# Optimization experiments

Measured on AMD Instinct MI355X. Metric: run time of the kernel, lower is better.

The kernel has to match this reference:

```python
import jax, jax.numpy as jnp
import numpy as np

N_NODES = 100000
N_EDGES = 1600000
D_IN = 128
D_OUT = 128


def setup_inputs() -> dict:
    key = jax.random.key(0)
    k_x, k_e, k_wl, k_bl, k_wr = jax.random.split(key, 5)
    x = jax.random.normal(k_x, (N_NODES, D_IN), dtype=jnp.float32)
    edge_index = jax.random.randint(k_e, (2, N_EDGES), 0, N_NODES, dtype=jnp.int64)
    s = 1.0 / np.sqrt(D_IN)
    W_l = jax.random.uniform(k_wl, (D_OUT, D_IN), minval=-s, maxval=s, dtype=jnp.float32)
    b_l = jax.random.uniform(k_bl, (D_OUT,), minval=-s, maxval=s, dtype=jnp.float32)
    W_r = jax.random.uniform(k_wr, (D_OUT, D_IN), minval=-s, maxval=s, dtype=jnp.float32)
    return {"x": x, "edge_index": edge_index, "W_l": W_l, "b_l": b_l, "W_r": W_r}


def reference(x, edge_index, W_l, b_l, W_r):
    # PyG SAGEConv with mean aggregation:
    #   out = lin_l(mean_{j in N(i)} x_j) + lin_r(x_i), followed by ReLU.
    src, dst = edge_index[0], edge_index[1]
    # gather source features [E, D_IN] and mean-aggregate at destinations
    msg_sum = jax.ops.segment_sum(x[src], dst, num_segments=N_NODES)  # [N, D_IN]
    deg = jax.ops.segment_sum(jnp.ones((edge_index.shape[1],), dtype=x.dtype), dst,
                              num_segments=N_NODES)  # [N]
    agg = msg_sum / jnp.maximum(deg, 1.0)[:, None]  # isolated nodes -> 0
    out = agg @ W_l.T + b_l + x @ W_r.T
    return jax.nn.relu(out)
```

## Files before the change

### kernel.cpp

```cpp
#include <hip/hip_runtime.h>
#include <hip/hip_bf16.h>
#include <cstddef>
#include <cstdint>

#define D 128
#define BCAP 262144
#define BCHUNK 4096
#define SLOTS 64
#define TILE 128
#define XBASE 8192
#define SBCAP 5120
#define GPGMAX 64

typedef __bf16 bf16x8 __attribute__((ext_vector_type(8)));
typedef float  f32x4  __attribute__((ext_vector_type(4)));
typedef float  f32x2  __attribute__((ext_vector_type(2)));

__device__ __forceinline__ unsigned int f2bf(float f) {
    unsigned int u = __float_as_uint(f);
    return (u + 0x7FFFu + ((u >> 16) & 1u)) >> 16;
}

__global__ __launch_bounds__(256) void bucketx_kernel(
    const int* __restrict__ ei, int E, int* __restrict__ bucketCnt,
    int2* __restrict__ buckets, int nbBucket, int nbX,
    const float4* __restrict__ x4, uint2* __restrict__ xb2,
    unsigned int* __restrict__ xg, int nq,
    const float* __restrict__ Wl, const float* __restrict__ Wr,
    const float* __restrict__ bl, unsigned short* __restrict__ bfrag,
    float* __restrict__ biasbuf)
{
    const int bid = blockIdx.x;
    if (bid >= nbBucket) {
        const int xi = bid - nbBucket;
        if (xi < nbX) {
            const int base = xi * 1024 + threadIdx.x;
            #pragma unroll
            for (int k = 0; k < 4; k++) {
                int i = base + k * 256;
                if (i < nq) {
                    float4 v = x4[i];
                    uint2 r;
                    r.x = f2bf(v.x) | (f2bf(v.y) << 16);
                    r.y = f2bf(v.z) | (f2bf(v.w) << 16);
                    xb2[i] = r;
                    int g = 0;
                    g = __builtin_amdgcn_cvt_pk_fp8_f32(v.x, v.y, g, false);
                    g = __builtin_amdgcn_cvt_pk_fp8_f32(v.z, v.w, g, true);
                    xg[(size_t)((i >> 5) + 1) * 32 + (i & 31)] = (unsigned int)g;
                }
            }
        } else {
            int f = (xi - nbX) * 256 + threadIdx.x;
            if (f < 4096) {
                int ct   = f >> 9;
                int q    = (f >> 6) & 7;
                int lane = f & 63;
                int o  = 16 * ct + (lane & 15);
                int kb = 32 * q + (lane >> 4) * 8;
                const float* s = (kb < 128) ? (Wl + (size_t)o * 128 + kb)
                                            : (Wr + (size_t)o * 128 + (kb - 128));
                uint4 u;
                u.x = f2bf(s[0]) | (f2bf(s[1]) << 16);
                u.y = f2bf(s[2]) | (f2bf(s[3]) << 16);
                u.z = f2bf(s[4]) | (f2bf(s[5]) << 16);
                u.w = f2bf(s[6]) | (f2bf(s[7]) << 16);
                reinterpret_cast<uint4*>(bfrag)[f] = u;
                if (f < 128) biasbuf[f] = bl[f];
                if (f < 32)  xg[f] = 0u;
            }
        }
        return;
    }
    __shared__ int cnt[8], base[8], pos[8];
    const int cb  = bid * BCHUNK;
    const int end = min(cb + BCHUNK, E);
    if (threadIdx.x < 8) { cnt[threadIdx.x] = 0; pos[threadIdx.x] = 0; }
    __syncthreads();
    int srcs[16], dsts[16];
    #pragma unroll
    for (int k = 0; k < 16; k++) {
        int e = cb + threadIdx.x + k * 256;
        bool v = e < end;
        srcs[k] = v ? ei[e] : 0;
        dsts[k] = v ? ei[E + e] : -1;
        if (v) atomicAdd(&cnt[(dsts[k] >> 8) & 7], 1);
    }
    __syncthreads();
    if (threadIdx.x < 8)
        base[threadIdx.x] = atomicAdd(&bucketCnt[threadIdx.x], cnt[threadIdx.x]);
    __syncthreads();
    #pragma unroll
    for (int k = 0; k < 16; k++) {
        if (dsts[k] >= 0) {
            int p = (dsts[k] >> 8) & 7;
            int o = base[p] + atomicAdd(&pos[p], 1);
            if (o < BCAP) buckets[(size_t)p * BCAP + o] = make_int2(srcs[k], dsts[k]);
        }
    }
}

__global__ __launch_bounds__(256) void granule_kernel(
    const int2* __restrict__ buckets, const int* __restrict__ bucketCnt,
    int* __restrict__ subCnt, unsigned int* __restrict__ sub, int GPG)
{
    __shared__ int cnt[GPGMAX], base[GPGMAX], posl[GPGMAX];
    const int p = blockIdx.x & 7;
    const int j = blockIdx.x >> 3;
    const int n = min(bucketCnt[p], BCAP);
    const int lo = j * 4096;
    if (lo >= n) return;
    const int hi = min(lo + 4096, n);
    for (int i = threadIdx.x; i < GPG; i += 256) { cnt[i] = 0; posl[i] = 0; }
    __syncthreads();
    const int2* B = buckets + (size_t)p * BCAP;
    int2 e[16]; int gi[16];
    #pragma unroll
    for (int k = 0; k < 16; k++) {
        int i = lo + threadIdx.x + k * 256;
        bool v = i < hi;
        e[k] = v ? B[i] : make_int2(0, 0);
        gi[k] = v ? (e[k].y >> 11) : -1;
        if (v) atomicAdd(&cnt[gi[k]], 1);
    }
    __syncthreads();
    for (int i = threadIdx.x; i < GPG; i += 256)
        base[i] = (cnt[i] > 0) ? atomicAdd(&subCnt[p * GPG + i], cnt[i]) : 0;
    __syncthreads();
    #pragma unroll
    for (int k = 0; k < 16; k++) {
        if (gi[k] >= 0) {
            int pos = base[gi[k]] + atomicAdd(&posl[gi[k]], 1);
            if (pos < SBCAP)
                sub[(size_t)(p * GPG + gi[k]) * SBCAP + pos] =
                    (unsigned int)(e[k].x + 1) | ((unsigned int)(e[k].y & 255) << 20);
        }
    }
}

__global__ __launch_bounds__(256) void csrg_kernel(
    const unsigned int* __restrict__ sub, const int* __restrict__ subCnt,
    int* __restrict__ csr, int* __restrict__ deg, int GPG, int N)
{
    __shared__ int lcnt[256];
    const int g  = blockIdx.x;
    const int p  = g & 7;
    const int gi = g >> 3;
    const int sb = p * GPG + gi;
    const int n  = min(subCnt[sb], SBCAP);
    lcnt[threadIdx.x] = 0;
    __syncthreads();
    const unsigned int* S = sub + (size_t)sb * SBCAP;
    const int nbase = g << 8;
    for (int i = threadIdx.x; i < n; i += 256) {
        unsigned int en = S[i];
        int d8  = (en >> 20) & 255;
        int pos = atomicAdd(&lcnt[d8], 1);
        if (pos < SLOTS)
            csr[(size_t)(nbase + d8) * SLOTS + pos] = (int)(en & 0xFFFFFu);
    }
    __syncthreads();
    int node = nbase + threadIdx.x;
    if (node < N) deg[node] = lcnt[threadIdx.x];
}

__device__ __forceinline__ void gather_issue(
    unsigned int (&vv)[16], int raw, int dl, int half, int sub,
    const unsigned int* __restrict__ xg)
{
    #pragma unroll
    for (int u = 0; u < 16; u++) {
        int slot = 2 * u + half;
        int s = (slot < dl) ? __shfl(raw, slot) : 0;
        vv[u] = xg[(size_t)s * 32 + sub];
    }
}

__device__ __forceinline__ void acc_reduce_write(
    const unsigned int (&vv)[16], int raw, int dl, int dT, int row,
    int half, int sub, const unsigned int* __restrict__ xg, unsigned int* lds)
{
    f32x2 a01 = {0.f, 0.f};
    f32x2 a23 = {0.f, 0.f};
    #pragma unroll
    for (int u = 0; u < 16; u++) {
        a01 += __builtin_amdgcn_cvt_pk_f32_fp8(vv[u], false);
        a23 += __builtin_amdgcn_cvt_pk_f32_fp8(vv[u], true);
    }
    if (dl > 32) {
        #pragma unroll
        for (int u = 0; u < 16; u++) {
            int slot = 32 + 2 * u + half;
            int s = (slot < dl) ? __shfl(raw, slot) : 0;
            unsigned int vt = xg[(size_t)s * 32 + sub];
            a01 += __builtin_amdgcn_cvt_pk_f32_fp8(vt, false);
            a23 += __builtin_amdgcn_cvt_pk_f32_fp8(vt, true);
        }
    }
    a01.x += __shfl_xor(a01.x, 32);
    a01.y += __shfl_xor(a01.y, 32);
    a23.x += __shfl_xor(a23.x, 32);
    a23.y += __shfl_xor(a23.y, 32);
    if (half == 0) {
        float inv = 1.0f / fmaxf((float)dT, 1.0f);
        int ch   = (sub >> 1) ^ (row & 7);
        int bofs = row * 64 + ch * 4 + (sub & 1) * 2;
        lds[bofs]     = f2bf(a01.x * inv) | (f2bf(a01.y * inv) << 16);
        lds[bofs + 1] = f2bf(a23.x * inv) | (f2bf(a23.y * inv) << 16);
    }
}

__global__ __launch_bounds__(512, 4) void gathformer_kernel(
    const int* __restrict__ deg_, const int* __restrict__ csr,
    const unsigned int* __restrict__ xg, const unsigned int* __restrict__ xb,
    const unsigned short* __restrict__ bfrag, const float* __restrict__ biasbuf,
    float* __restrict__ out, int N)
{
    __shared__ unsigned int lds[2 * TILE * 64];

    const int w    = threadIdx.x >> 6;
    const int lane = threadIdx.x & 63;
    const int sub  = lane & 31;
    const int half = lane >> 5;
    const int node0 = blockIdx.x * TILE;

    uint4 xs[4];
    const uint4* xb4 = reinterpret_cast<const uint4*>(xb);
    #pragma unroll
    for (int k = 0; k < 4; k++) {
        int idx = k * 512 + (int)threadIdx.x;
        int row = idx >> 4;
        int gr  = min(node0 + row, N - 1);
        xs[k] = xb4[(size_t)gr * 16 + (idx & 15)];
    }

    const int nb0 = node0 + w * 16;
    int degv = 0;
    if (lane < 16) {
        int nd = nb0 + lane;
        if (nd < N) degv = deg_[nd];
    }
    int r0 = csr[(size_t)min(nb0 + 0, N - 1) * SLOTS + lane];
    int r1 = csr[(size_t)min(nb0 + 1, N - 1) * SLOTS + lane];
    int r2 = csr[(size_t)min(nb0 + 2, N - 1) * SLOTS + lane];

    #pragma unroll
    for (int k = 0; k < 4; k++) {
        int idx = k * 512 + (int)threadIdx.x;
        int row = idx >> 4;
        int cw  = (idx & 15) ^ (row & 7);
        *reinterpret_cast<uint4*>(&lds[XBASE + row * 64 + cw * 4]) = xs[k];
    }

    unsigned int vA[16], vB[16];
    int dl0 = min(__shfl(degv, 0), SLOTS);
    gather_issue(vA, r0, dl0, half, sub, xg);
    #pragma unroll
    for (int i = 0; i < 16; i += 2) {
        int dl1 = min(__shfl(degv, i + 1), SLOTS);
        gather_issue(vB, r1, dl1, half, sub, xg);
        int r3 = (i + 3 < 16) ? csr[(size_t)min(nb0 + i + 3, N - 1) * SLOTS + lane] : 0;
        int dT0 = __shfl(degv, i);
        acc_reduce_write(vA, r0, dl0, dT0, w * 16 + i, half, sub, xg, lds);
        dl0 = (i + 2 < 16) ? min(__shfl(degv, i + 2), SLOTS) : 0;
        if (i + 2 < 16) gather_issue(vA, r2, dl0, half, sub, xg);
        int r4 = (i + 4 < 16) ? csr[(size_t)min(nb0 + i + 4, N - 1) * SLOTS + lane] : 0;
        int dT1 = __shfl(degv, i + 1);
        acc_reduce_write(vB, r1, dl1, dT1, w * 16 + i + 1, half, sub, xg, lds);
        r0 = r2; r1 = r3; r2 = r4;
    }

    const int quad = lane >> 4;
    const int r15  = lane & 15;
    bf16x8 bw[8];
    #pragma unroll
    for (int q = 0; q < 8; q++)
        bw[q] = reinterpret_cast<const bf16x8*>(bfrag)[(w * 8 + q) * 64 + lane];
    const float bias = biasbuf[16 * w + r15];
    const int col = 16 * w + r15;

    __syncthreads();

    #pragma unroll 2
    for (int mt = 0; mt < 8; mt++) {
        int rowbase = node0 + mt * 16;
        if (rowbase >= N) break;
        f32x4 acc = {0.f, 0.f, 0.f, 0.f};
        const int r     = mt * 16 + r15;
        const int rbase = r * 64;
        const int rx    = r & 7;
        #pragma unroll
        for (int q = 0; q < 4; q++) {
            int ch = (quad + 4 * q) ^ rx;
            bf16x8 a = *reinterpret_cast<const bf16x8*>(&lds[rbase + ch * 4]);
            acc = __builtin_amdgcn_mfma_f32_16x16x32_bf16(a, bw[q], acc, 0, 0, 0);
        }
        #pragma unroll
        for (int q = 0; q < 4; q++) {
            int ch = (quad + 4 * q) ^ rx;
            bf16x8 a = *reinterpret_cast<const bf16x8*>(&lds[XBASE + rbase + ch * 4]);
            acc = __builtin_amdgcn_mfma_f32_16x16x32_bf16(a, bw[4 + q], acc, 0, 0, 0);
        }
        #pragma unroll
        for (int rr = 0; rr < 4; rr++) {
            int orow = rowbase + quad * 4 + rr;
            if (orow < N)
                out[(size_t)orow * D + col] = fmaxf(acc[rr] + bias, 0.0f);
        }
    }
}

extern "C" void kernel_launch(void* const* d_in, const int* in_sizes, int n_in,
                              void* d_out, int out_size, void* d_ws, size_t ws_size,
                              hipStream_t stream)
{
    const float* x  = (const float*)d_in[0];
    const int*   ei = (const int*)d_in[1];
    const float* Wl = (const float*)d_in[2];
    const float* bl = (const float*)d_in[3];
    const float* Wr = (const float*)d_in[4];
    float* out = (float*)d_out;

    const int nodes = in_sizes[0] / D;
    const int E     = in_sizes[1] / 2;
    const int NG    = (nodes + 255) >> 8;
    const int GPG   = (NG + 7) >> 3;

    int* deg         = (int*)d_ws;
    unsigned int* xg = (unsigned int*)(deg + nodes);
    int* csr         = (int*)(xg + (size_t)(nodes + 1) * 32);
    unsigned int* xb = (unsigned int*)(csr + (size_t)nodes * SLOTS);
    unsigned short* bfrag = (unsigned short*)(xb + (size_t)nodes * 64);
    float* biasbuf   = (float*)(bfrag + 4096 * 8);
    int* bucketCnt   = (int*)(biasbuf + 128);
    int* subCnt      = bucketCnt + 8;
    int2* buckets    = (int2*)d_out;
    unsigned int* sub = (unsigned int*)((char*)d_out + (size_t)8 * BCAP * 8);

    hipMemsetAsync(bucketCnt, 0, (size_t)(8 + 8 * GPG) * sizeof(int), stream);

    const int nbBucket = (E + BCHUNK - 1) / BCHUNK;
    const int nq  = nodes * 32;
    const int nbX = (nq + 1023) / 1024;
    bucketx_kernel<<<nbBucket + nbX + 16, 256, 0, stream>>>(
        ei, E, bucketCnt, buckets, nbBucket, nbX,
        (const float4*)x, (uint2*)xb, xg, nq, Wl, Wr, bl, bfrag, biasbuf);

    const int PB = (BCAP + 4095) / 4096;
    granule_kernel<<<8 * PB, 256, 0, stream>>>(buckets, bucketCnt, subCnt, sub, GPG);

    csrg_kernel<<<NG, 256, 0, stream>>>(sub, subCnt, csr, deg, GPG, nodes);

    gathformer_kernel<<<(nodes + TILE - 1) / TILE, 512, 0, stream>>>(
        deg, csr, xg, xb, bfrag, biasbuf, out, nodes);
}
```

Before: 221.5 us.

## Replace three-pass bucketed CSR build with direct global-atomic scatter

```diff
diff --git a/kernel.cpp b/kernel.cpp
--- a/kernel.cpp
+++ b/kernel.cpp
@@ -4,13 +4,10 @@
 #include <cstdint>
 
 #define D 128
-#define BCAP 262144
 #define BCHUNK 4096
 #define SLOTS 64
 #define TILE 128
 #define XBASE 8192
-#define SBCAP 5120
-#define GPGMAX 64
 
 typedef __bf16 bf16x8 __attribute__((ext_vector_type(8)));
 typedef float  f32x4  __attribute__((ext_vector_type(4)));
@@ -21,9 +18,9 @@
     return (u + 0x7FFFu + ((u >> 16) & 1u)) >> 16;
 }
 
-__global__ __launch_bounds__(256) void bucketx_kernel(
-    const int* __restrict__ ei, int E, int* __restrict__ bucketCnt,
-    int2* __restrict__ buckets, int nbBucket, int nbX,
+__global__ __launch_bounds__(256) void scatterx_kernel(
+    const int* __restrict__ ei, int E, int* __restrict__ deg,
+    int* __restrict__ csr, int nbScat, int nbX,
     const float4* __restrict__ x4, uint2* __restrict__ xb2,
     unsigned int* __restrict__ xg, int nq,
     const float* __restrict__ Wl, const float* __restrict__ Wr,
@@ -31,8 +28,8 @@
     float* __restrict__ biasbuf)
 {
     const int bid = blockIdx.x;
-    if (bid >= nbBucket) {
-        const int xi = bid - nbBucket;
+    if (bid >= nbScat) {
+        const int xi = bid - nbScat;
         if (xi < nbX) {
             const int base = xi * 1024 + threadIdx.x;
             #pragma unroll
@@ -72,96 +69,23 @@
         }
         return;
     }
-    __shared__ int cnt[8], base[8], pos[8];
-    const int cb  = bid * BCHUNK;
-    const int end = min(cb + BCHUNK, E);
-    if (threadIdx.x < 8) { cnt[threadIdx.x] = 0; pos[threadIdx.x] = 0; }
-    __syncthreads();
+    const int cb = bid * BCHUNK;
     int srcs[16], dsts[16];
     #pragma unroll
     for (int k = 0; k < 16; k++) {
         int e = cb + threadIdx.x + k * 256;
-        bool v = e < end;
+        bool v = e < E;
         srcs[k] = v ? ei[e] : 0;
         dsts[k] = v ? ei[E + e] : -1;
-        if (v) atomicAdd(&cnt[(dsts[k] >> 8) & 7], 1);
-    }
-    __syncthreads();
-    if (threadIdx.x < 8)
-        base[threadIdx.x] = atomicAdd(&bucketCnt[threadIdx.x], cnt[threadIdx.x]);
-    __syncthreads();
+    }
     #pragma unroll
     for (int k = 0; k < 16; k++) {
         if (dsts[k] >= 0) {
-            int p = (dsts[k] >> 8) & 7;
-            int o = base[p] + atomicAdd(&pos[p], 1);
-            if (o < BCAP) buckets[(size_t)p * BCAP + o] = make_int2(srcs[k], dsts[k]);
-        }
-    }
-}
-
-__global__ __launch_bounds__(256) void granule_kernel(
-    const int2* __restrict__ buckets, const int* __restrict__ bucketCnt,
-    int* __restrict__ subCnt, unsigned int* __restrict__ sub, int GPG)
-{
-    __shared__ int cnt[GPGMAX], base[GPGMAX], posl[GPGMAX];
-    const int p = blockIdx.x & 7;
-    const int j = blockIdx.x >> 3;
-    const int n = min(bucketCnt[p], BCAP);
-    const int lo = j * 4096;
-    if (lo >= n) return;
-    const int hi = min(lo + 4096, n);
-    for (int i = threadIdx.x; i < GPG; i += 256) { cnt[i] = 0; posl[i] = 0; }
-    __syncthreads();
-    const int2* B = buckets + (size_t)p * BCAP;
-    int2 e[16]; int gi[16];
-    #pragma unroll
-    for (int k = 0; k < 16; k++) {
-        int i = lo + threadIdx.x + k * 256;
-        bool v = i < hi;
-        e[k] = v ? B[i] : make_int2(0, 0);
-        gi[k] = v ? (e[k].y >> 11) : -1;
-        if (v) atomicAdd(&cnt[gi[k]], 1);
-    }
-    __syncthreads();
-    for (int i = threadIdx.x; i < GPG; i += 256)
-        base[i] = (cnt[i] > 0) ? atomicAdd(&subCnt[p * GPG + i], cnt[i]) : 0;
-    __syncthreads();
-    #pragma unroll
-    for (int k = 0; k < 16; k++) {
-        if (gi[k] >= 0) {
-            int pos = base[gi[k]] + atomicAdd(&posl[gi[k]], 1);
-            if (pos < SBCAP)
-                sub[(size_t)(p * GPG + gi[k]) * SBCAP + pos] =
-                    (unsigned int)(e[k].x + 1) | ((unsigned int)(e[k].y & 255) << 20);
-        }
-    }
-}
-
-__global__ __launch_bounds__(256) void csrg_kernel(
-    const unsigned int* __restrict__ sub, const int* __restrict__ subCnt,
-    int* __restrict__ csr, int* __restrict__ deg, int GPG, int N)
-{
-    __shared__ int lcnt[256];
-    const int g  = blockIdx.x;
-    const int p  = g & 7;
-    const int gi = g >> 3;
-    const int sb = p * GPG + gi;
-    const int n  = min(subCnt[sb], SBCAP);
-    lcnt[threadIdx.x] = 0;
-    __syncthreads();
-    const unsigned int* S = sub + (size_t)sb * SBCAP;
-    const int nbase = g << 8;
-    for (int i = threadIdx.x; i < n; i += 256) {
-        unsigned int en = S[i];
-        int d8  = (en >> 20) & 255;
-        int pos = atomicAdd(&lcnt[d8], 1);
-        if (pos < SLOTS)
-            csr[(size_t)(nbase + d8) * SLOTS + pos] = (int)(en & 0xFFFFFu);
-    }
-    __syncthreads();
-    int node = nbase + threadIdx.x;
-    if (node < N) deg[node] = lcnt[threadIdx.x];
+            int pos = atomicAdd(&deg[dsts[k]], 1);
+            if (pos < SLOTS)
+                csr[(size_t)dsts[k] * SLOTS + pos] = srcs[k] + 1;
+        }
+    }
 }
 
 __device__ __forceinline__ void gather_issue(
@@ -323,8 +247,6 @@
 
     const int nodes = in_sizes[0] / D;
     const int E     = in_sizes[1] / 2;
-    const int NG    = (nodes + 255) >> 8;
-    const int GPG   = (NG + 7) >> 3;
 
     int* deg         = (int*)d_ws;
     unsigned int* xg = (unsigned int*)(deg + nodes);
@@ -332,24 +254,15 @@
     unsigned int* xb = (unsigned int*)(csr + (size_t)nodes * SLOTS);
     unsigned short* bfrag = (unsigned short*)(xb + (size_t)nodes * 64);
     float* biasbuf   = (float*)(bfrag + 4096 * 8);
-    int* bucketCnt   = (int*)(biasbuf + 128);
-    int* subCnt      = bucketCnt + 8;
-    int2* buckets    = (int2*)d_out;
-    unsigned int* sub = (unsigned int*)((char*)d_out + (size_t)8 * BCAP * 8);
-
-    hipMemsetAsync(bucketCnt, 0, (size_t)(8 + 8 * GPG) * sizeof(int), stream);
-
-    const int nbBucket = (E + BCHUNK - 1) / BCHUNK;
+
+    hipMemsetAsync(deg, 0, (size_t)nodes * sizeof(int), stream);
+
+    const int nbScat = (E + BCHUNK - 1) / BCHUNK;
     const int nq  = nodes * 32;
     const int nbX = (nq + 1023) / 1024;
-    bucketx_kernel<<<nbBucket + nbX + 16, 256, 0, stream>>>(
-        ei, E, bucketCnt, buckets, nbBucket, nbX,
+    scatterx_kernel<<<nbScat + nbX + 16, 256, 0, stream>>>(
+        ei, E, deg, csr, nbScat, nbX,
         (const float4*)x, (uint2*)xb, xg, nq, Wl, Wr, bl, bfrag, biasbuf);
-
-    const int PB = (BCAP + 4095) / 4096;
-    granule_kernel<<<8 * PB, 256, 0, stream>>>(buckets, bucketCnt, subCnt, sub, GPG);
-
-    csrg_kernel<<<NG, 256, 0, stream>>>(sub, subCnt, csr, deg, GPG, nodes);
 
     gathformer_kernel<<<(nodes + TILE - 1) / TILE, 512, 0, stream>>>(
         deg, csr, xg, xb, bfrag, biasbuf, out, nodes);
```

New measurement: 312.5 us. 41.0% more time.
